# Kernel optimization log

Measured on AMD Instinct MI355X. Metric: run time of the kernel, lower is better.

The kernel has to match this reference:

```python
import jax, jax.numpy as jnp
import numpy as np

K = 20
EPS = 1e-5


def knn_idx(x, k):
    # x: (B, N, C) -> (B, N, k) indices of k nearest neighbors (incl. self)
    xx = jnp.sum(x * x, axis=-1, keepdims=True)           # (B,N,1)
    inner = -2.0 * jnp.einsum('bnc,bmc->bnm', x, x)        # (B,N,N)
    pd = -xx - inner - jnp.swapaxes(xx, 1, 2)              # negative sq dist
    _, idx = jax.lax.top_k(pd, k)                          # (B,N,k)
    return idx


def get_graph_feature(x, k=K):
    B, N, C = x.shape
    idx = knn_idx(x, k)                                    # (B,N,k)
    # gather neighbor features per batch
    feature = jax.vmap(lambda xb, ib: xb[ib])(x, idx)      # (B,N,k,C)
    xe = jnp.broadcast_to(x[:, :, None, :], (B, N, k, C))  # (B,N,k,C)
    f = jnp.concatenate([feature - xe, xe], axis=3)        # (B,N,k,2C)
    return jnp.transpose(f, (0, 3, 1, 2))                  # (B,2C,N,k)


def conv1x1(x, W, b):
    # x: (B,Cin,N,k), W: (Cout,Cin)
    return jnp.einsum('bcnk,oc->bonk', x, W) + b[None, :, None, None]


def batchnorm(x, gamma, beta):
    # training-mode BN over (B,N,k) per channel, biased variance (torch default)
    mean = jnp.mean(x, axis=(0, 2, 3), keepdims=True)
    var = jnp.var(x, axis=(0, 2, 3), keepdims=True)
    xhat = (x - mean) * jax.lax.rsqrt(var + EPS)
    return xhat * gamma[None, :, None, None] + beta[None, :, None, None]


def setup_inputs() -> dict:
    key = jax.random.key(0)
    ks = jax.random.split(key, 10)
    B, N, C = 4, 4096, 3
    x = jax.random.normal(ks[0], (B, N, C), dtype=jnp.float32)
    W1 = jax.random.normal(ks[1], (64, 2 * C), dtype=jnp.float32) * 0.1
    b1 = jnp.zeros((64,), jnp.float32)
    g1 = jnp.ones((64,), jnp.float32)
    be1 = jnp.zeros((64,), jnp.float32)
    W2 = jax.random.normal(ks[2], (128, 64), dtype=jnp.float32) * 0.1
    b2 = jnp.zeros((128,), jnp.float32)
    g2 = jnp.ones((128,), jnp.float32)
    be2 = jnp.zeros((128,), jnp.float32)
    W3 = jax.random.normal(ks[3], (128, 128), dtype=jnp.float32) * 0.1
    b3 = jnp.zeros((128,), jnp.float32)
    g3 = jnp.ones((128,), jnp.float32)
    be3 = jnp.zeros((128,), jnp.float32)
    return {"x": x, "W1": W1, "b1": b1, "g1": g1, "be1": be1,
            "W2": W2, "b2": b2, "g2": g2, "be2": be2,
            "W3": W3, "b3": b3, "g3": g3, "be3": be3}


def reference(x, W1, b1, g1, be1, W2, b2, g2, be2, W3, b3, g3, be3):
    f = get_graph_feature(x, K)                  # (B,6,N,k)
    h = jax.nn.relu(batchnorm(conv1x1(f, W1, b1), g1, be1))
    h = jax.nn.relu(batchnorm(conv1x1(h, W2, b2), g2, be2))
    h = batchnorm(conv1x1(h, W3, b3), g3, be3)
    return jnp.max(h, axis=-1)                   # (B,128,N)
```

## Files before the change

### kernel.cpp

```cpp
#include <hip/hip_runtime.h>


typedef __attribute__((ext_vector_type(8)))  short short8;
typedef __attribute__((ext_vector_type(4)))  float floatx4;

#define BATCH 4
#define NPTS  4096
#define KNN   20
#define BN_   (BATCH*NPTS)
#define CNT   (BATCH*NPTS*KNN)

__device__ __forceinline__ unsigned short f2bf(float f) {
  unsigned u = __float_as_uint(f);
  unsigned r = u + 0x7FFFu + ((u >> 16) & 1u);
  return (unsigned short)(r >> 16);
}

__device__ __forceinline__ short8 pack8(float a, float b, float c, float d,
                                        float e, float f, float g, float h) {
  short8 r;
  r[0]=(short)f2bf(a); r[1]=(short)f2bf(b); r[2]=(short)f2bf(c); r[3]=(short)f2bf(d);
  r[4]=(short)f2bf(e); r[5]=(short)f2bf(f); r[6]=(short)f2bf(g); r[7]=(short)f2bf(h);
  return r;
}

__device__ __forceinline__ unsigned mono(float f) {
  unsigned u = __float_as_uint(f);
  return u ^ ((unsigned)((int)u >> 31) | 0x80000000u);
}

__global__ void pf_prep(const float* __restrict__ x, float4* __restrict__ xp,
                        float* __restrict__ stats) {
  int pt = blockIdx.x * 256 + threadIdx.x;
  float x0 = x[pt*3+0], x1 = x[pt*3+1], x2 = x[pt*3+2];
  float xx = x0*x0 + x1*x1 + x2*x2;
  xp[pt] = make_float4(x0, x1, x2, xx);
  if (blockIdx.x == 0)
    for (int i = threadIdx.x; i < 640; i += 256) stats[i] = 0.0f;
}

__device__ __forceinline__ float sort_take20th(float v, int lane) {
  #pragma unroll
  for (int k = 2; k <= 64; k <<= 1) {
    #pragma unroll
    for (int j = k >> 1; j >= 1; j >>= 1) {
      float o = __shfl_xor(v, j);
      bool keepmax = (((lane & j) == 0) == ((lane & k) == 0));
      v = keepmax ? fmaxf(v, o) : fminf(v, o);
    }
  }
  return __shfl(v, 19);
}

__device__ __forceinline__ unsigned long long sort64_desc(unsigned long long v,
                                                          int lane) {
  #pragma unroll
  for (int k = 2; k <= 64; k <<= 1) {
    #pragma unroll
    for (int j = k >> 1; j >= 1; j >>= 1) {
      unsigned long long o = __shfl_xor(v, j);
      bool keepmax = (((lane & j) == 0) == ((lane & k) == 0));
      unsigned long long hi = v > o ? v : o;
      unsigned long long lo = v > o ? o : v;
      v = keepmax ? hi : lo;
    }
  }
  return v;
}

__global__ __launch_bounds__(256) void pf_knn(const float4* __restrict__ xp,
                                              int* __restrict__ idxb) {
  __shared__ unsigned long long lst[8][128];
  __shared__ int lcnt[8];
  const int tid  = threadIdx.x;
  const int lane = tid & 63;
  const int w    = tid >> 6;
  const int b    = blockIdx.x >> 9;
  const int nb   = (blockIdx.x & 511) * 8 + w * 2;
  const float4* xb = xp + b * NPTS;

  float4 q0 = xb[nb], q1 = xb[nb + 1];

  float mx0 = -3.0e38f, mx1 = -3.0e38f;
  for (int j0 = 0; j0 < NPTS; j0 += 64) {
    float4 c = xb[j0 + lane];
    float d0 = fmaf(q0.x,c.x, fmaf(q0.y,c.y, q0.z*c.z));
    float d1 = fmaf(q1.x,c.x, fmaf(q1.y,c.y, q1.z*c.z));
    mx0 = fmaxf(mx0, fmaf(2.f,d0,-q0.w) - c.w);
    mx1 = fmaxf(mx1, fmaf(2.f,d1,-q1.w) - c.w);
  }
  float T0 = sort_take20th(mx0, lane);
  float T1 = sort_take20th(mx1, lane);

  if (lane < 2) lcnt[w*2 + lane] = 0;
  __syncthreads();

  for (int j0 = 0; j0 < NPTS; j0 += 64) {
    float4 c = xb[j0 + lane];
    float d0 = fmaf(q0.x,c.x, fmaf(q0.y,c.y, q0.z*c.z));
    float d1 = fmaf(q1.x,c.x, fmaf(q1.y,c.y, q1.z*c.z));
    float p0 = fmaf(2.f,d0,-q0.w) - c.w;
    float p1 = fmaf(2.f,d1,-q1.w) - c.w;
    unsigned long long keybase = (unsigned long long)(4095 - (j0 + lane));
    if (p0 >= T0) {
      int o = atomicAdd(&lcnt[w*2+0], 1);
      if (o < 128) lst[w*2+0][o] = ((unsigned long long)mono(p0) << 32) | keybase;
    }
    if (p1 >= T1) {
      int o = atomicAdd(&lcnt[w*2+1], 1);
      if (o < 128) lst[w*2+1][o] = ((unsigned long long)mono(p1) << 32) | keybase;
    }
  }

  #pragma unroll 1
  for (int i = 0; i < 2; ++i) {
    const int li = w*2 + i;
    const int cn = lcnt[li];
    const int outbase = (b * NPTS + nb + i) * KNN;
    if (cn <= 64) {
      unsigned long long v = (lane < cn) ? lst[li][lane] : 0ull;
      v = sort64_desc(v, lane);
      if (lane < KNN) idxb[outbase + lane] = 4095 - (int)(v & 0xFFFFFFFFull);
    } else if (cn <= 128) {
      unsigned long long e0 = lst[li][lane];
      unsigned long long e1 = (lane + 64 < cn) ? lst[li][lane + 64] : 0ull;
      #pragma unroll 1
      for (int r = 0; r < KNN; ++r) {
        unsigned long long m = e0 > e1 ? e0 : e1;
        #pragma unroll
        for (int o = 32; o; o >>= 1) {
          unsigned long long t = __shfl_xor(m, o);
          m = t > m ? t : m;
        }
        if (lane == 0) idxb[outbase + r] = 4095 - (int)(m & 0xFFFFFFFFull);
        if (e0 == m) e0 = 0ull; else if (e1 == m) e1 = 0ull;
      }
    } else {
      const float4 qq = (i == 0) ? q0 : q1;
      unsigned long long prev = ~0ull;
      #pragma unroll 1
      for (int r = 0; r < KNN; ++r) {
        unsigned long long best = 0ull;
        for (int j0 = 0; j0 < NPTS; j0 += 64) {
          float4 c = xb[j0 + lane];
          float dd = fmaf(qq.x,c.x, fmaf(qq.y,c.y, qq.z*c.z));
          float pd = fmaf(2.f,dd,-qq.w) - c.w;
          unsigned long long key = ((unsigned long long)mono(pd) << 32) |
                                   (unsigned long long)(4095 - (j0 + lane));
          if (key < prev && key > best) best = key;
        }
        #pragma unroll
        for (int o = 32; o; o >>= 1) {
          unsigned long long t = __shfl_xor(best, o);
          best = t > best ? t : best;
        }
        if (lane == 0) idxb[outbase + r] = 4095 - (int)(best & 0xFFFFFFFFull);
        prev = best;
      }
    }
  }
}

__global__ __launch_bounds__(256) void pf_stats1(
    const float4* __restrict__ xp, const int* __restrict__ idxb,
    const float* __restrict__ W1, const float* __restrict__ b1,
    float* __restrict__ gs1, float* __restrict__ gq1) {
  __shared__ float S[64], Q[64];
  const int tid = threadIdx.x;
  const int c = tid & 63, slice = tid >> 6;
  if (tid < 64) { S[tid] = 0.f; Q[tid] = 0.f; }
  __syncthreads();
  const float wa0=W1[c*6+0], wa1=W1[c*6+1], wa2=W1[c*6+2];
  const float wb0=W1[c*6+3], wb1=W1[c*6+4], wb2=W1[c*6+5];
  const float bb = b1[c];
  float s = 0.f, q = 0.f;
  int ptbase = (blockIdx.x * 4 + slice) * 4;
  for (int u = 0; u < 4; ++u) {
    int pt = ptbase + u;
    float4 xi = xp[pt];
    int ib = (pt >> 12) << 12;
    for (int kk = 0; kk < KNN; ++kk) {
      int j = idxb[pt*KNN + kk];
      float4 xj = xp[ib + j];
      float y = bb;
      y = fmaf(wa0, xj.x - xi.x, y);
      y = fmaf(wa1, xj.y - xi.y, y);
      y = fmaf(wa2, xj.z - xi.z, y);
      y = fmaf(wb0, xi.x, y);
      y = fmaf(wb1, xi.y, y);
      y = fmaf(wb2, xi.z, y);
      s += y; q = fmaf(y, y, q);
    }
  }
  atomicAdd(&S[c], s); atomicAdd(&Q[c], q);
  __syncthreads();
  if (tid < 64) { atomicAdd(&gs1[tid], S[tid]); atomicAdd(&gq1[tid], Q[tid]); }
}

__global__ void pf_affine(const float* __restrict__ gs, const float* __restrict__ gq,
                          const float* __restrict__ gamma, const float* __restrict__ beta,
                          const float* __restrict__ bconv, int foldb, int C,
                          float* __restrict__ sc, float* __restrict__ sh) {
  int c = threadIdx.x;
  if (c < C) {
    const float inv = 1.0f / (float)CNT;
    float mean = gs[c] * inv;
    float var  = gq[c] * inv - mean * mean;
    float s = gamma[c] * rsqrtf(var + 1e-5f);
    float shift = beta[c] - mean * s;
    if (foldb) shift = fmaf(s, bconv[c], shift);
    sc[c] = s; sh[c] = shift;
  }
}

__global__ __launch_bounds__(256, 2) void pf_stats2(
    const float4* __restrict__ xp, const int* __restrict__ idxb,
    const float* __restrict__ W1, const float* __restrict__ sc1e,
    const float* __restrict__ sh1e, const float* __restrict__ W2,
    const float* __restrict__ b2,
    float* __restrict__ gs2, float* __restrict__ gq2) {
  __shared__ __align__(16) float4 XI[32];
  __shared__ __align__(16) float4 XJ[32];
  __shared__ __align__(16) unsigned short H1[32][72];
  __shared__ float SS[128], SQ[128];

  const int tid = threadIdx.x;
  const int lane = tid & 63, w = tid >> 6;
  const int chalf = w & 1, rh = w >> 1;
  const int l15 = lane & 15, quad = lane >> 4;
  const int pt0 = blockIdx.x * 32;

  if (tid < 128) { SS[tid] = 0.f; SQ[tid] = 0.f; }
  if (tid < 32)  XI[tid] = xp[pt0 + tid];

  short8 w1f[2];
  #pragma unroll
  for (int t = 0; t < 2; ++t) {
    short8 f = {0,0,0,0,0,0,0,0};
    if (quad == 0) {
      const float* p = W1 + (32*chalf + 16*t + l15) * 6;
      f = pack8(p[0],p[1],p[2],p[3],p[4],p[5],0.f,0.f);
    }
    w1f[t] = f;
  }
  float a1[2], s1[2];
  #pragma unroll
  for (int t = 0; t < 2; ++t) {
    int c = 32*chalf + 16*t + l15;
    a1[t] = sc1e[c]; s1[t] = sh1e[c];
  }
  short8 w2f[2][4];
  #pragma unroll
  for (int ks = 0; ks < 2; ++ks)
    #pragma unroll
    for (int t = 0; t < 4; ++t) {
      const float* p = W2 + (64*chalf + 16*t + l15) * 64 + 32*ks + quad*8;
      w2f[ks][t] = pack8(p[0],p[1],p[2],p[3],p[4],p[5],p[6],p[7]);
    }
  float bb2[4];
  #pragma unroll
  for (int t = 0; t < 4; ++t) bb2[t] = b2[64*chalf + 16*t + l15];

  float sum[4] = {0,0,0,0}, sq[4] = {0,0,0,0};

  for (int kk = 0; kk < KNN; ++kk) {
    if (tid < 32) {
      int pt = pt0 + tid;
      XJ[tid] = xp[((pt >> 12) << 12) + idxb[pt*KNN + kk]];
    }
    __syncthreads();
    short8 af = {0,0,0,0,0,0,0,0};
    if (quad == 0) {
      float4 xi = XI[rh*16 + l15];
      float4 xj = XJ[rh*16 + l15];
      af = pack8(xj.x-xi.x, xj.y-xi.y, xj.z-xi.z, xi.x, xi.y, xi.z, 0.f, 0.f);
    }
    floatx4 acc1[2] = {{0,0,0,0},{0,0,0,0}};
    #pragma unroll
    for (int t = 0; t < 2; ++t)
      acc1[t] = __builtin_amdgcn_mfma_f32_16x16x32_bf16(af, w1f[t], acc1[t], 0,0,0);
    #pragma unroll
    for (int t = 0; t < 2; ++t) {
      int c = 32*chalf + 16*t + l15;
      #pragma unroll
      for (int r = 0; r < 4; ++r) {
        float h = fmaxf(fmaf(a1[t], acc1[t][r], s1[t]), 0.f);
        H1[rh*16 + quad*4 + r][c] = f2bf(h);
      }
    }
    __syncthreads();
    floatx4 acc2[4] = {{0,0,0,0},{0,0,0,0},{0,0,0,0},{0,0,0,0}};
    #pragma unroll
    for (int ks = 0; ks < 2; ++ks) {
      short8 a = *(const short8*)&H1[rh*16 + l15][ks*32 + quad*8];
      #pragma unroll
      for (int t = 0; t < 4; ++t)
        acc2[t] = __builtin_amdgcn_mfma_f32_16x16x32_bf16(a, w2f[ks][t], acc2[t], 0,0,0);
    }
    #pragma unroll
    for (int t = 0; t < 4; ++t)
      #pragma unroll
      for (int r = 0; r < 4; ++r) {
        float v = acc2[t][r] + bb2[t];
        sum[t] += v; sq[t] = fmaf(v, v, sq[t]);
      }
  }
  #pragma unroll
  for (int t = 0; t < 4; ++t) {
    float s = sum[t], z = sq[t];
    s += __shfl_xor(s, 16); z += __shfl_xor(z, 16);
    s += __shfl_xor(s, 32); z += __shfl_xor(z, 32);
    if (quad == 0) {
      int c = 64*chalf + 16*t + l15;
      atomicAdd(&SS[c], s); atomicAdd(&SQ[c], z);
    }
  }
  __syncthreads();
  if (tid < 128) { atomicAdd(&gs2[tid], SS[tid]); atomicAdd(&gq2[tid], SQ[tid]); }
}

__global__ __launch_bounds__(256, 2) void pf_main(
    const float4* __restrict__ xp, const int* __restrict__ idxb,
    const float* __restrict__ W1, const float* __restrict__ sc1e,
    const float* __restrict__ sh1e, const float* __restrict__ W2,
    const float* __restrict__ sc2e, const float* __restrict__ shm2,
    const float* __restrict__ W3, const float* __restrict__ b3,
    float* __restrict__ gs3, float* __restrict__ gq3,
    float* __restrict__ maxv) {
  __shared__ __align__(16) float4 XI[32];
  __shared__ __align__(16) float4 XJ[32];
  __shared__ __align__(16) unsigned short H1[32][72];
  __shared__ __align__(16) unsigned short H2[32][136];
  __shared__ float SS[128], SQ[128];

  const int tid = threadIdx.x;
  const int lane = tid & 63, w = tid >> 6;
  const int chalf = w & 1, rh = w >> 1;
  const int l15 = lane & 15, quad = lane >> 4;
  const int pt0 = blockIdx.x * 32;

  if (tid < 128) { SS[tid] = 0.f; SQ[tid] = 0.f; }
  if (tid < 32)  XI[tid] = xp[pt0 + tid];

  short8 w1f[2];
  #pragma unroll
  for (int t = 0; t < 2; ++t) {
    short8 f = {0,0,0,0,0,0,0,0};
    if (quad == 0) {
      const float* p = W1 + (32*chalf + 16*t + l15) * 6;
      f = pack8(p[0],p[1],p[2],p[3],p[4],p[5],0.f,0.f);
    }
    w1f[t] = f;
  }
  float a1[2], s1[2];
  #pragma unroll
  for (int t = 0; t < 2; ++t) {
    int c = 32*chalf + 16*t + l15;
    a1[t] = sc1e[c]; s1[t] = sh1e[c];
  }
  short8 w2f[2][4];
  #pragma unroll
  for (int ks = 0; ks < 2; ++ks)
    #pragma unroll
    for (int t = 0; t < 4; ++t) {
      const float* p = W2 + (64*chalf + 16*t + l15) * 64 + 32*ks + quad*8;
      w2f[ks][t] = pack8(p[0],p[1],p[2],p[3],p[4],p[5],p[6],p[7]);
    }
  float a2[4], s2[4], bb3[4];
  #pragma unroll
  for (int t = 0; t < 4; ++t) {
    int c = 64*chalf + 16*t + l15;
    a2[t] = sc2e[c]; s2[t] = shm2[c]; bb3[t] = b3[c];
  }
  short8 w3f[4][4];
  #pragma unroll
  for (int ks = 0; ks < 4; ++ks)
    #pragma unroll
    for (int t = 0; t < 4; ++t) {
      const float* p = W3 + (64*chalf + 16*t + l15) * 128 + 32*ks + quad*8;
      w3f[ks][t] = pack8(p[0],p[1],p[2],p[3],p[4],p[5],p[6],p[7]);
    }

  float sum[4] = {0,0,0,0}, sq[4] = {0,0,0,0};
  float mx[4][4];
  #pragma unroll
  for (int t = 0; t < 4; ++t)
    #pragma unroll
    for (int r = 0; r < 4; ++r) mx[t][r] = -3.0e38f;

  for (int kk = 0; kk < KNN; ++kk) {
    if (tid < 32) {
      int pt = pt0 + tid;
      XJ[tid] = xp[((pt >> 12) << 12) + idxb[pt*KNN + kk]];
    }
    __syncthreads();
    short8 af = {0,0,0,0,0,0,0,0};
    if (quad == 0) {
      float4 xi = XI[rh*16 + l15];
      float4 xj = XJ[rh*16 + l15];
      af = pack8(xj.x-xi.x, xj.y-xi.y, xj.z-xi.z, xi.x, xi.y, xi.z, 0.f, 0.f);
    }
    floatx4 acc1[2] = {{0,0,0,0},{0,0,0,0}};
    #pragma unroll
    for (int t = 0; t < 2; ++t)
      acc1[t] = __builtin_amdgcn_mfma_f32_16x16x32_bf16(af, w1f[t], acc1[t], 0,0,0);
    #pragma unroll
    for (int t = 0; t < 2; ++t) {
      int c = 32*chalf + 16*t + l15;
      #pragma unroll
      for (int r = 0; r < 4; ++r) {
        float h = fmaxf(fmaf(a1[t], acc1[t][r], s1[t]), 0.f);
        H1[rh*16 + quad*4 + r][c] = f2bf(h);
      }
    }
    __syncthreads();
    floatx4 acc2[4] = {{0,0,0,0},{0,0,0,0},{0,0,0,0},{0,0,0,0}};
    #pragma unroll
    for (int ks = 0; ks < 2; ++ks) {
      short8 a = *(const short8*)&H1[rh*16 + l15][ks*32 + quad*8];
      #pragma unroll
      for (int t = 0; t < 4; ++t)
        acc2[t] = __builtin_amdgcn_mfma_f32_16x16x32_bf16(a, w2f[ks][t], acc2[t], 0,0,0);
    }
    #pragma unroll
    for (int t = 0; t < 4; ++t) {
      int c = 64*chalf + 16*t + l15;
      #pragma unroll
      for (int r = 0; r < 4; ++r) {
        float h = fmaxf(fmaf(a2[t], acc2[t][r], s2[t]), 0.f);
        H2[rh*16 + quad*4 + r][c] = f2bf(h);
      }
    }
    __syncthreads();
    floatx4 acc3[4] = {{0,0,0,0},{0,0,0,0},{0,0,0,0},{0,0,0,0}};
    #pragma unroll
    for (int ks = 0; ks < 4; ++ks) {
      short8 a = *(const short8*)&H2[rh*16 + l15][ks*32 + quad*8];
      #pragma unroll
      for (int t = 0; t < 4; ++t)
        acc3[t] = __builtin_amdgcn_mfma_f32_16x16x32_bf16(a, w3f[ks][t], acc3[t], 0,0,0);
    }
    #pragma unroll
    for (int t = 0; t < 4; ++t)
      #pragma unroll
      for (int r = 0; r < 4; ++r) {
        float v = acc3[t][r] + bb3[t];
        sum[t] += v; sq[t] = fmaf(v, v, sq[t]);
        mx[t][r] = fmaxf(mx[t][r], v);
      }
  }
  #pragma unroll
  for (int t = 0; t < 4; ++t) {
    int c = 64*chalf + 16*t + l15;
    #pragma unroll
    for (int r = 0; r < 4; ++r) {
      int row = rh*16 + quad*4 + r;
      maxv[(pt0 + row)*128 + c] = mx[t][r];
    }
  }
  #pragma unroll
  for (int t = 0; t < 4; ++t) {
    float s = sum[t], z = sq[t];
    s += __shfl_xor(s, 16); z += __shfl_xor(z, 16);
    s += __shfl_xor(s, 32); z += __shfl_xor(z, 32);
    if (quad == 0) {
      int c = 64*chalf + 16*t + l15;
      atomicAdd(&SS[c], s); atomicAdd(&SQ[c], z);
    }
  }
  __syncthreads();
  if (tid < 128) { atomicAdd(&gs3[tid], SS[tid]); atomicAdd(&gq3[tid], SQ[tid]); }
}

__global__ __launch_bounds__(256) void pf_out(
    const float* __restrict__ maxv, const float* __restrict__ sc3,
    const float* __restrict__ sh3, float* __restrict__ out) {
  __shared__ float T[128][65];
  __shared__ float SC[128], SH[128];
  const int tid = threadIdx.x;
  const int b  = blockIdx.x >> 6;
  const int n0 = (blockIdx.x & 63) * 64;
  if (tid < 128) { SC[tid] = sc3[tid]; SH[tid] = sh3[tid]; }
  __syncthreads();
  const float4* mv4 = (const float4*)maxv;
  #pragma unroll
  for (int r = 0; r < 8; ++r) {
    int fid = r * 256 + tid;
    int nl = fid >> 5, c4 = fid & 31;
    float4 v = mv4[(b*NPTS + n0 + nl)*32 + c4];
    int c = c4 * 4;
    T[c+0][nl] = fmaf(SC[c+0], v.x, SH[c+0]);
    T[c+1][nl] = fmaf(SC[c+1], v.y, SH[c+1]);
    T[c+2][nl] = fmaf(SC[c+2], v.z, SH[c+2]);
    T[c+3][nl] = fmaf(SC[c+3], v.w, SH[c+3]);
  }
  __syncthreads();
  #pragma unroll
  for (int r = 0; r < 8; ++r) {
    int fid = r * 256 + tid;
    int c = fid >> 4, nq = fid & 15;
    float4 o;
    o.x = T[c][nq*4+0]; o.y = T[c][nq*4+1];
    o.z = T[c][nq*4+2]; o.w = T[c][nq*4+3];
    *(float4*)(out + (size_t)b*128*NPTS + (size_t)c*NPTS + n0 + nq*4) = o;
  }
}

extern "C" void kernel_launch(void* const* d_in, const int* in_sizes, int n_in,
                              void* d_out, int out_size, void* d_ws, size_t ws_size,
                              hipStream_t stream) {
  const float* x   = (const float*)d_in[0];
  const float* W1  = (const float*)d_in[1];
  const float* b1  = (const float*)d_in[2];
  const float* g1  = (const float*)d_in[3];
  const float* be1 = (const float*)d_in[4];
  const float* W2  = (const float*)d_in[5];
  const float* b2  = (const float*)d_in[6];
  const float* g2  = (const float*)d_in[7];
  const float* be2 = (const float*)d_in[8];
  const float* W3  = (const float*)d_in[9];
  const float* b3  = (const float*)d_in[10];
  const float* g3  = (const float*)d_in[11];
  const float* be3 = (const float*)d_in[12];
  float* out = (float*)d_out;

  char* p = (char*)d_ws;
  float4* xp  = (float4*)p;            p += (size_t)BN_ * 16;
  int*    idxb= (int*)p;               p += (size_t)BN_ * KNN * 4;
  float*  stats = (float*)p;           p += 640 * 4;
  float*  aff   = (float*)p;           p += 640 * 4;
  float*  maxv  = (float*)p;

  float *gs1 = stats,       *gq1 = stats + 64;
  float *gs2 = stats + 128, *gq2 = stats + 256;
  float *gs3 = stats + 384, *gq3 = stats + 512;
  float *sc1e = aff,        *sh1e = aff + 64;
  float *sc2e = aff + 128,  *shm2 = aff + 256;
  float *sc3  = aff + 384,  *sh3  = aff + 512;

  pf_prep  <<<64,   256, 0, stream>>>(x, xp, stats);
  pf_knn   <<<2048, 256, 0, stream>>>(xp, idxb);
  pf_stats1<<<1024, 256, 0, stream>>>(xp, idxb, W1, b1, gs1, gq1);
  pf_affine<<<1,    64,  0, stream>>>(gs1, gq1, g1, be1, b1, 1, 64, sc1e, sh1e);
  pf_stats2<<<512,  256, 0, stream>>>(xp, idxb, W1, sc1e, sh1e, W2, b2, gs2, gq2);
  pf_affine<<<1,    128, 0, stream>>>(gs2, gq2, g2, be2, b2, 1, 128, sc2e, shm2);
  pf_main  <<<512,  256, 0, stream>>>(xp, idxb, W1, sc1e, sh1e, W2, sc2e, shm2,
                                      W3, b3, gs3, gq3, maxv);
  pf_affine<<<1,    128, 0, stream>>>(gs3, gq3, g3, be3, b3, 0, 128, sc3, sh3);
  pf_out   <<<256,  256, 0, stream>>>(maxv, sc3, sh3, out);
}
```

Before: 250.6 us.

## Compute BN1 stats from input moments, split k across blocks, fold BN scales

Layer-1 BatchNorm statistics now come from the 27 first and second moments of the 6-dim edge features, combined with W1 in a tiny affine kernel, replacing the per-channel gather pass. The stats2 and main kernels work on 16 points per block instead of 32 and can split the 20 neighbours over two blocks, each writing a partial max plane that pf_out merges. This raises the block count and occupancy. They also fold the BN scale into the bf16 weights, start the accumulators at the shift or bias, and double-buffer the neighbour gather. The risks are rounding from pre-scaled bf16 weights and extra maxv traffic when the workspace allows the split.

Result: slower. 328.3 us (+31.0%).

```diff
diff --git a/kernel.cpp b/kernel.cpp
--- a/kernel.cpp
+++ b/kernel.cpp
@@ -161,40 +161,70 @@
   }
 }
 
-__global__ __launch_bounds__(256) void pf_stats1(
+__global__ __launch_bounds__(256) void pf_mom(
     const float4* __restrict__ xp, const int* __restrict__ idxb,
-    const float* __restrict__ W1, const float* __restrict__ b1,
-    float* __restrict__ gs1, float* __restrict__ gq1) {
-  __shared__ float S[64], Q[64];
+    float* __restrict__ mom) {
+  __shared__ float M[27];
   const int tid = threadIdx.x;
-  const int c = tid & 63, slice = tid >> 6;
-  if (tid < 64) { S[tid] = 0.f; Q[tid] = 0.f; }
-  __syncthreads();
-  const float wa0=W1[c*6+0], wa1=W1[c*6+1], wa2=W1[c*6+2];
-  const float wb0=W1[c*6+3], wb1=W1[c*6+4], wb2=W1[c*6+5];
-  const float bb = b1[c];
-  float s = 0.f, q = 0.f;
-  int ptbase = (blockIdx.x * 4 + slice) * 4;
-  for (int u = 0; u < 4; ++u) {
-    int pt = ptbase + u;
-    float4 xi = xp[pt];
-    int ib = (pt >> 12) << 12;
-    for (int kk = 0; kk < KNN; ++kk) {
-      int j = idxb[pt*KNN + kk];
-      float4 xj = xp[ib + j];
-      float y = bb;
-      y = fmaf(wa0, xj.x - xi.x, y);
-      y = fmaf(wa1, xj.y - xi.y, y);
-      y = fmaf(wa2, xj.z - xi.z, y);
-      y = fmaf(wb0, xi.x, y);
-      y = fmaf(wb1, xi.y, y);
-      y = fmaf(wb2, xi.z, y);
-      s += y; q = fmaf(y, y, q);
-    }
-  }
-  atomicAdd(&S[c], s); atomicAdd(&Q[c], q);
-  __syncthreads();
-  if (tid < 64) { atomicAdd(&gs1[tid], S[tid]); atomicAdd(&gq1[tid], Q[tid]); }
+  if (tid < 27) M[tid] = 0.f;
+  __syncthreads();
+  const int gid = blockIdx.x * 256 + tid;
+  const int pt = gid >> 1;
+  const int kk0 = (gid & 1) * 10;
+  const float4 xi = xp[pt];
+  const int ib = pt & ~(NPTS - 1);
+  float a[27];
+  #pragma unroll
+  for (int i = 0; i < 27; ++i) a[i] = 0.f;
+  #pragma unroll 1
+  for (int u = 0; u < 10; ++u) {
+    int j = idxb[pt*KNN + kk0 + u];
+    float4 xj = xp[ib + j];
+    float f[6] = {xj.x - xi.x, xj.y - xi.y, xj.z - xi.z, xi.x, xi.y, xi.z};
+    int idx = 6;
+    #pragma unroll
+    for (int i1 = 0; i1 < 6; ++i1) {
+      a[i1] += f[i1];
+      #pragma unroll
+      for (int i2 = i1; i2 < 6; ++i2) { a[idx] = fmaf(f[i1], f[i2], a[idx]); ++idx; }
+    }
+  }
+  #pragma unroll
+  for (int i = 0; i < 27; ++i) atomicAdd(&M[i], a[i]);
+  __syncthreads();
+  if (tid < 27) atomicAdd(&mom[tid], M[tid]);
+}
+
+__global__ void pf_affine1m(const float* __restrict__ mom,
+                            const float* __restrict__ W1, const float* __restrict__ b1,
+                            const float* __restrict__ g1, const float* __restrict__ be1,
+                            float* __restrict__ sc, float* __restrict__ sh) {
+  int c = threadIdx.x;
+  float wv[6];
+  #pragma unroll
+  for (int i = 0; i < 6; ++i) wv[i] = W1[c*6 + i];
+  float b = b1[c];
+  float S1 = b * (float)CNT;
+  float Q  = b * b * (float)CNT;
+  int idx = 6;
+  #pragma unroll
+  for (int i = 0; i < 6; ++i) {
+    float m1 = mom[i];
+    S1 += wv[i] * m1;
+    Q  += 2.0f * b * wv[i] * m1;
+    #pragma unroll
+    for (int j = i; j < 6; ++j) {
+      float coef = (i == j) ? 1.0f : 2.0f;
+      Q += coef * wv[i] * wv[j] * mom[idx];
+      ++idx;
+    }
+  }
+  const float inv = 1.0f / (float)CNT;
+  float mean = S1 * inv;
+  float var  = Q * inv - mean * mean;
+  float s = g1[c] * rsqrtf(var + 1e-5f);
+  sc[c] = s;
+  sh[c] = be1[c] - mean * s + s * b;
 }
 
 __global__ void pf_affine(const float* __restrict__ gs, const float* __restrict__ gq,
@@ -213,105 +243,96 @@
   }
 }
 
-__global__ __launch_bounds__(256, 2) void pf_stats2(
+__global__ __launch_bounds__(256, 4) void pf_stats2(
     const float4* __restrict__ xp, const int* __restrict__ idxb,
     const float* __restrict__ W1, const float* __restrict__ sc1e,
     const float* __restrict__ sh1e, const float* __restrict__ W2,
-    const float* __restrict__ b2,
+    const float* __restrict__ b2, int kshift, int kpb,
     float* __restrict__ gs2, float* __restrict__ gq2) {
-  __shared__ __align__(16) float4 XI[32];
-  __shared__ __align__(16) float4 XJ[32];
-  __shared__ __align__(16) unsigned short H1[32][72];
+  __shared__ __align__(16) float4 XI[16];
+  __shared__ __align__(16) float4 XJ[2][16];
+  __shared__ __align__(16) unsigned short H1[2][16][72];
   __shared__ float SS[128], SQ[128];
 
   const int tid = threadIdx.x;
   const int lane = tid & 63, w = tid >> 6;
-  const int chalf = w & 1, rh = w >> 1;
   const int l15 = lane & 15, quad = lane >> 4;
-  const int pt0 = blockIdx.x * 32;
+  const int pg = blockIdx.x >> kshift;
+  const int ks0 = blockIdx.x & ((1 << kshift) - 1);
+  const int kk0 = ks0 * kpb;
+  const int pt0 = pg * 16;
+  const int ib = pt0 & ~(NPTS - 1);
 
   if (tid < 128) { SS[tid] = 0.f; SQ[tid] = 0.f; }
-  if (tid < 32)  XI[tid] = xp[pt0 + tid];
-
-  short8 w1f[2];
+  if (tid < 16) XI[tid] = xp[pt0 + tid];
+  if (tid < 16) XJ[0][tid] = xp[ib + idxb[(pt0 + tid)*KNN + kk0]];
+
+  const int c1 = 16*w + l15;
+  const float s1 = sh1e[c1];
+  short8 w1f = {0,0,0,0,0,0,0,0};
+  {
+    float a1 = sc1e[c1];
+    if (quad == 0) {
+      const float* p = W1 + c1*6;
+      w1f = pack8(p[0]*a1,p[1]*a1,p[2]*a1,p[3]*a1,p[4]*a1,p[5]*a1,0.f,0.f);
+    }
+  }
+  short8 w2f[2][2];
+  float bb2[2];
   #pragma unroll
   for (int t = 0; t < 2; ++t) {
-    short8 f = {0,0,0,0,0,0,0,0};
-    if (quad == 0) {
-      const float* p = W1 + (32*chalf + 16*t + l15) * 6;
-      f = pack8(p[0],p[1],p[2],p[3],p[4],p[5],0.f,0.f);
-    }
-    w1f[t] = f;
-  }
-  float a1[2], s1[2];
-  #pragma unroll
-  for (int t = 0; t < 2; ++t) {
-    int c = 32*chalf + 16*t + l15;
-    a1[t] = sc1e[c]; s1[t] = sh1e[c];
-  }
-  short8 w2f[2][4];
-  #pragma unroll
-  for (int ks = 0; ks < 2; ++ks)
-    #pragma unroll
-    for (int t = 0; t < 4; ++t) {
-      const float* p = W2 + (64*chalf + 16*t + l15) * 64 + 32*ks + quad*8;
-      w2f[ks][t] = pack8(p[0],p[1],p[2],p[3],p[4],p[5],p[6],p[7]);
-    }
-  float bb2[4];
-  #pragma unroll
-  for (int t = 0; t < 4; ++t) bb2[t] = b2[64*chalf + 16*t + l15];
-
-  float sum[4] = {0,0,0,0}, sq[4] = {0,0,0,0};
-
-  for (int kk = 0; kk < KNN; ++kk) {
-    if (tid < 32) {
-      int pt = pt0 + tid;
-      XJ[tid] = xp[((pt >> 12) << 12) + idxb[pt*KNN + kk]];
-    }
-    __syncthreads();
+    int c = 32*w + 16*t + l15;
+    bb2[t] = b2[c];
+    #pragma unroll
+    for (int ksl = 0; ksl < 2; ++ksl) {
+      const float* p = W2 + c*64 + 32*ksl + quad*8;
+      w2f[ksl][t] = pack8(p[0],p[1],p[2],p[3],p[4],p[5],p[6],p[7]);
+    }
+  }
+
+  float sum[2] = {0,0}, sq[2] = {0,0};
+  __syncthreads();
+
+  for (int it = 0; it < kpb; ++it) {
+    const int cur = it & 1;
     short8 af = {0,0,0,0,0,0,0,0};
     if (quad == 0) {
-      float4 xi = XI[rh*16 + l15];
-      float4 xj = XJ[rh*16 + l15];
+      float4 xi = XI[l15];
+      float4 xj = XJ[cur][l15];
       af = pack8(xj.x-xi.x, xj.y-xi.y, xj.z-xi.z, xi.x, xi.y, xi.z, 0.f, 0.f);
     }
-    floatx4 acc1[2] = {{0,0,0,0},{0,0,0,0}};
+    if (tid < 16 && it + 1 < kpb)
+      XJ[1-cur][tid] = xp[ib + idxb[(pt0 + tid)*KNN + kk0 + it + 1]];
+    floatx4 acc1 = {s1, s1, s1, s1};
+    acc1 = __builtin_amdgcn_mfma_f32_16x16x32_bf16(af, w1f, acc1, 0,0,0);
+    #pragma unroll
+    for (int r = 0; r < 4; ++r)
+      H1[cur][quad*4 + r][c1] = f2bf(fmaxf(acc1[r], 0.f));
+    __syncthreads();
+    floatx4 acc2[2] = {{bb2[0],bb2[0],bb2[0],bb2[0]},
+                       {bb2[1],bb2[1],bb2[1],bb2[1]}};
+    #pragma unroll
+    for (int ksl = 0; ksl < 2; ++ksl) {
+      short8 a = *(const short8*)&H1[cur][l15][ksl*32 + quad*8];
+      #pragma unroll
+      for (int t = 0; t < 2; ++t)
+        acc2[t] = __builtin_amdgcn_mfma_f32_16x16x32_bf16(a, w2f[ksl][t], acc2[t], 0,0,0);
+    }
     #pragma unroll
     for (int t = 0; t < 2; ++t)
-      acc1[t] = __builtin_amdgcn_mfma_f32_16x16x32_bf16(af, w1f[t], acc1[t], 0,0,0);
-    #pragma unroll
-    for (int t = 0; t < 2; ++t) {
-      int c = 32*chalf + 16*t + l15;
       #pragma unroll
       for (int r = 0; r < 4; ++r) {
-        float h = fmaxf(fmaf(a1[t], acc1[t][r], s1[t]), 0.f);
-        H1[rh*16 + quad*4 + r][c] = f2bf(h);
-      }
-    }
-    __syncthreads();
-    floatx4 acc2[4] = {{0,0,0,0},{0,0,0,0},{0,0,0,0},{0,0,0,0}};
-    #pragma unroll
-    for (int ks = 0; ks < 2; ++ks) {
-      short8 a = *(const short8*)&H1[rh*16 + l15][ks*32 + quad*8];
-      #pragma unroll
-      for (int t = 0; t < 4; ++t)
-        acc2[t] = __builtin_amdgcn_mfma_f32_16x16x32_bf16(a, w2f[ks][t], acc2[t], 0,0,0);
-    }
-    #pragma unroll
-    for (int t = 0; t < 4; ++t)
-      #pragma unroll
-      for (int r = 0; r < 4; ++r) {
-        float v = acc2[t][r] + bb2[t];
+        float v = acc2[t][r];
         sum[t] += v; sq[t] = fmaf(v, v, sq[t]);
       }
   }
   #pragma unroll
-  for (int t = 0; t < 4; ++t) {
+  for (int t = 0; t < 2; ++t) {
     float s = sum[t], z = sq[t];
     s += __shfl_xor(s, 16); z += __shfl_xor(z, 16);
     s += __shfl_xor(s, 32); z += __shfl_xor(z, 32);
     if (quad == 0) {
-      int c = 64*chalf + 16*t + l15;
+      int c = 32*w + 16*t + l15;
       atomicAdd(&SS[c], s); atomicAdd(&SQ[c], z);
     }
   }
@@ -319,152 +340,145 @@
   if (tid < 128) { atomicAdd(&gs2[tid], SS[tid]); atomicAdd(&gq2[tid], SQ[tid]); }
 }
 
-__global__ __launch_bounds__(256, 2) void pf_main(
+__global__ __launch_bounds__(256, 4) void pf_main(
     const float4* __restrict__ xp, const int* __restrict__ idxb,
     const float* __restrict__ W1, const float* __restrict__ sc1e,
     const float* __restrict__ sh1e, const float* __restrict__ W2,
     const float* __restrict__ sc2e, const float* __restrict__ shm2,
     const float* __restrict__ W3, const float* __restrict__ b3,
+    int kshift, int kpb,
     float* __restrict__ gs3, float* __restrict__ gq3,
     float* __restrict__ maxv) {
-  __shared__ __align__(16) float4 XI[32];
-  __shared__ __align__(16) float4 XJ[32];
-  __shared__ __align__(16) unsigned short H1[32][72];
-  __shared__ __align__(16) unsigned short H2[32][136];
+  __shared__ __align__(16) float4 XI[16];
+  __shared__ __align__(16) float4 XJ[2][16];
+  __shared__ __align__(16) unsigned short H1[16][72];
+  __shared__ __align__(16) unsigned short H2[16][136];
   __shared__ float SS[128], SQ[128];
 
   const int tid = threadIdx.x;
   const int lane = tid & 63, w = tid >> 6;
-  const int chalf = w & 1, rh = w >> 1;
   const int l15 = lane & 15, quad = lane >> 4;
-  const int pt0 = blockIdx.x * 32;
+  const int pg = blockIdx.x >> kshift;
+  const int ks0 = blockIdx.x & ((1 << kshift) - 1);
+  const int kk0 = ks0 * kpb;
+  const int pt0 = pg * 16;
+  const int ib = pt0 & ~(NPTS - 1);
 
   if (tid < 128) { SS[tid] = 0.f; SQ[tid] = 0.f; }
-  if (tid < 32)  XI[tid] = xp[pt0 + tid];
-
-  short8 w1f[2];
+  if (tid < 16) XI[tid] = xp[pt0 + tid];
+  if (tid < 16) XJ[0][tid] = xp[ib + idxb[(pt0 + tid)*KNN + kk0]];
+
+  const int c1 = 16*w + l15;
+  const float s1 = sh1e[c1];
+  short8 w1f = {0,0,0,0,0,0,0,0};
+  {
+    float a1 = sc1e[c1];
+    if (quad == 0) {
+      const float* p = W1 + c1*6;
+      w1f = pack8(p[0]*a1,p[1]*a1,p[2]*a1,p[3]*a1,p[4]*a1,p[5]*a1,0.f,0.f);
+    }
+  }
+  short8 w2f[2][2];
+  float s2v[2];
   #pragma unroll
   for (int t = 0; t < 2; ++t) {
-    short8 f = {0,0,0,0,0,0,0,0};
-    if (quad == 0) {
-      const float* p = W1 + (32*chalf + 16*t + l15) * 6;
-      f = pack8(p[0],p[1],p[2],p[3],p[4],p[5],0.f,0.f);
-    }
-    w1f[t] = f;
-  }
-  float a1[2], s1[2];
+    int c = 32*w + 16*t + l15;
+    float a2 = sc2e[c];
+    s2v[t] = shm2[c];
+    #pragma unroll
+    for (int ksl = 0; ksl < 2; ++ksl) {
+      const float* p = W2 + c*64 + 32*ksl + quad*8;
+      w2f[ksl][t] = pack8(p[0]*a2,p[1]*a2,p[2]*a2,p[3]*a2,p[4]*a2,p[5]*a2,p[6]*a2,p[7]*a2);
+    }
+  }
+  short8 w3f[4][2];
+  float bb3[2];
   #pragma unroll
   for (int t = 0; t < 2; ++t) {
-    int c = 32*chalf + 16*t + l15;
-    a1[t] = sc1e[c]; s1[t] = sh1e[c];
-  }
-  short8 w2f[2][4];
-  #pragma unroll
-  for (int ks = 0; ks < 2; ++ks)
-    #pragma unroll
-    for (int t = 0; t < 4; ++t) {
-      const float* p = W2 + (64*chalf + 16*t + l15) * 64 + 32*ks + quad*8;
-      w2f[ks][t] = pack8(p[0],p[1],p[2],p[3],p[4],p[5],p[6],p[7]);
-    }
-  float a2[4], s2[4], bb3[4];
-  #pragma unroll
-  for (int t = 0; t < 4; ++t) {
-    int c = 64*chalf + 16*t + l15;
-    a2[t] = sc2e[c]; s2[t] = shm2[c]; bb3[t] = b3[c];
-  }
-  short8 w3f[4][4];
-  #pragma unroll
-  for (int ks = 0; ks < 4; ++ks)
-    #pragma unroll
-    for (int t = 0; t < 4; ++t) {
-      const float* p = W3 + (64*chalf + 16*t + l15) * 128 + 32*ks + quad*8;
-      w3f[ks][t] = pack8(p[0],p[1],p[2],p[3],p[4],p[5],p[6],p[7]);
-    }
-
-  float sum[4] = {0,0,0,0}, sq[4] = {0,0,0,0};
-  float mx[4][4];
-  #pragma unroll
-  for (int t = 0; t < 4; ++t)
+    int c = 32*w + 16*t + l15;
+    bb3[t] = b3[c];
+    #pragma unroll
+    for (int ksl = 0; ksl < 4; ++ksl) {
+      const float* p = W3 + c*128 + 32*ksl + quad*8;
+      w3f[ksl][t] = pack8(p[0],p[1],p[2],p[3],p[4],p[5],p[6],p[7]);
+    }
+  }
+
+  float sum[2] = {0,0}, sq[2] = {0,0};
+  float mx[2][4];
+  #pragma unroll
+  for (int t = 0; t < 2; ++t)
     #pragma unroll
     for (int r = 0; r < 4; ++r) mx[t][r] = -3.0e38f;
 
-  for (int kk = 0; kk < KNN; ++kk) {
-    if (tid < 32) {
-      int pt = pt0 + tid;
-      XJ[tid] = xp[((pt >> 12) << 12) + idxb[pt*KNN + kk]];
-    }
-    __syncthreads();
+  __syncthreads();
+
+  for (int it = 0; it < kpb; ++it) {
+    const int cur = it & 1;
     short8 af = {0,0,0,0,0,0,0,0};
     if (quad == 0) {
-      float4 xi = XI[rh*16 + l15];
-      float4 xj = XJ[rh*16 + l15];
+      float4 xi = XI[l15];
+      float4 xj = XJ[cur][l15];
       af = pack8(xj.x-xi.x, xj.y-xi.y, xj.z-xi.z, xi.x, xi.y, xi.z, 0.f, 0.f);
     }
-    floatx4 acc1[2] = {{0,0,0,0},{0,0,0,0}};
+    if (tid < 16 && it + 1 < kpb)
+      XJ[1-cur][tid] = xp[ib + idxb[(pt0 + tid)*KNN + kk0 + it + 1]];
+    floatx4 acc1 = {s1, s1, s1, s1};
+    acc1 = __builtin_amdgcn_mfma_f32_16x16x32_bf16(af, w1f, acc1, 0,0,0);
+    #pragma unroll
+    for (int r = 0; r < 4; ++r)
+      H1[quad*4 + r][c1] = f2bf(fmaxf(acc1[r], 0.f));
+    __syncthreads();
+    floatx4 acc2[2] = {{s2v[0],s2v[0],s2v[0],s2v[0]},
+                       {s2v[1],s2v[1],s2v[1],s2v[1]}};
+    #pragma unroll
+    for (int ksl = 0; ksl < 2; ++ksl) {
+      short8 a = *(const short8*)&H1[l15][ksl*32 + quad*8];
+      #pragma unroll
+      for (int t = 0; t < 2; ++t)
+        acc2[t] = __builtin_amdgcn_mfma_f32_16x16x32_bf16(a, w2f[ksl][t], acc2[t], 0,0,0);
+    }
+    #pragma unroll
+    for (int t = 0; t < 2; ++t) {
+      int c = 32*w + 16*t + l15;
+      #pragma unroll
+      for (int r = 0; r < 4; ++r)
+        H2[quad*4 + r][c] = f2bf(fmaxf(acc2[t][r], 0.f));
+    }
+    __syncthreads();
+    floatx4 acc3[2] = {{bb3[0],bb3[0],bb3[0],bb3[0]},
+                       {bb3[1],bb3[1],bb3[1],bb3[1]}};
+    #pragma unroll
+    for (int ksl = 0; ksl < 4; ++ksl) {
+      short8 a = *(const short8*)&H2[l15][ksl*32 + quad*8];
+      #pragma unroll
+      for (int t = 0; t < 2; ++t)
+        acc3[t] = __builtin_amdgcn_mfma_f32_16x16x32_bf16(a, w3f[ksl][t], acc3[t], 0,0,0);
+    }
     #pragma unroll
     for (int t = 0; t < 2; ++t)
-      acc1[t] = __builtin_amdgcn_mfma_f32_16x16x32_bf16(af, w1f[t], acc1[t], 0,0,0);
-    #pragma unroll
-    for (int t = 0; t < 2; ++t) {
-      int c = 32*chalf + 16*t + l15;
       #pragma unroll
       for (int r = 0; r < 4; ++r) {
-        float h = fmaxf(fmaf(a1[t], acc1[t][r], s1[t]), 0.f);
-        H1[rh*16 + quad*4 + r][c] = f2bf(h);
-      }
-    }
-    __syncthreads();
-    floatx4 acc2[4] = {{0,0,0,0},{0,0,0,0},{0,0,0,0},{0,0,0,0}};
-    #pragma unroll
-    for (int ks = 0; ks < 2; ++ks) {
-      short8 a = *(const short8*)&H1[rh*16 + l15][ks*32 + quad*8];
-      #pragma unroll
-      for (int t = 0; t < 4; ++t)
-        acc2[t] = __builtin_amdgcn_mfma_f32_16x16x32_bf16(a, w2f[ks][t], acc2[t], 0,0,0);
-    }
-    #pragma unroll
-    for (int t = 0; t < 4; ++t) {
-      int c = 64*chalf + 16*t + l15;
-      #pragma unroll
-      for (int r = 0; r < 4; ++r) {
-        float h = fmaxf(fmaf(a2[t], acc2[t][r], s2[t]), 0.f);
-        H2[rh*16 + quad*4 + r][c] = f2bf(h);
-      }
-    }
-    __syncthreads();
-    floatx4 acc3[4] = {{0,0,0,0},{0,0,0,0},{0,0,0,0},{0,0,0,0}};
-    #pragma unroll
-    for (int ks = 0; ks < 4; ++ks) {
-      short8 a = *(const short8*)&H2[rh*16 + l15][ks*32 + quad*8];
-      #pragma unroll
-      for (int t = 0; t < 4; ++t)
-        acc3[t] = __builtin_amdgcn_mfma_f32_16x16x32_bf16(a, w3f[ks][t], acc3[t], 0,0,0);
-    }
-    #pragma unroll
-    for (int t = 0; t < 4; ++t)
-      #pragma unroll
-      for (int r = 0; r < 4; ++r) {
-        float v = acc3[t][r] + bb3[t];
+        float v = acc3[t][r];
         sum[t] += v; sq[t] = fmaf(v, v, sq[t]);
         mx[t][r] = fmaxf(mx[t][r], v);
       }
   }
-  #pragma unroll
-  for (int t = 0; t < 4; ++t) {
-    int c = 64*chalf + 16*t + l15;
-    #pragma unroll
-    for (int r = 0; r < 4; ++r) {
-      int row = rh*16 + quad*4 + r;
-      maxv[(pt0 + row)*128 + c] = mx[t][r];
-    }
-  }
-  #pragma unroll
-  for (int t = 0; t < 4; ++t) {
+  float* mp = maxv + (size_t)ks0 * BN_ * 128;
+  #pragma unroll
+  for (int t = 0; t < 2; ++t) {
+    int c = 32*w + 16*t + l15;
+    #pragma unroll
+    for (int r = 0; r < 4; ++r)
+      mp[(pt0 + quad*4 + r)*128 + c] = mx[t][r];
+  }
+  #pragma unroll
+  for (int t = 0; t < 2; ++t) {
     float s = sum[t], z = sq[t];
     s += __shfl_xor(s, 16); z += __shfl_xor(z, 16);
     s += __shfl_xor(s, 32); z += __shfl_xor(z, 32);
     if (quad == 0) {
-      int c = 64*chalf + 16*t + l15;
+      int c = 32*w + 16*t + l15;
       atomicAdd(&SS[c], s); atomicAdd(&SQ[c], z);
     }
   }
@@ -473,8 +487,9 @@
 }
 
 __global__ __launch_bounds__(256) void pf_out(
-    const float* __restrict__ maxv, const float* __restrict__ sc3,
-    const float* __restrict__ sh3, float* __restrict__ out) {
+    const float* __restrict__ maxv, int nspl,
+    const float* __restrict__ sc3, const float* __restrict__ sh3,
+    float* __restrict__ out) {
   __shared__ float T[128][65];
   __shared__ float SC[128], SH[128];
   const int tid = threadIdx.x;
@@ -488,6 +503,11 @@
     int fid = r * 256 + tid;
     int nl = fid >> 5, c4 = fid & 31;
     float4 v = mv4[(b*NPTS + n0 + nl)*32 + c4];
+    if (nspl == 2) {
+      float4 v2 = mv4[524288 + (b*NPTS + n0 + nl)*32 + c4];
+      v.x = fmaxf(v.x, v2.x); v.y = fmaxf(v.y, v2.y);
+      v.z = fmaxf(v.z, v2.z); v.w = fmaxf(v.w, v2.w);
+    }
     int c = c4 * 4;
     T[c+0][nl] = fmaf(SC[c+0], v.x, SH[c+0]);
     T[c+1][nl] = fmaf(SC[c+1], v.y, SH[c+1]);
@@ -525,27 +545,35 @@
   float* out = (float*)d_out;
 
   char* p = (char*)d_ws;
-  float4* xp  = (float4*)p;            p += (size_t)BN_ * 16;
-  int*    idxb= (int*)p;               p += (size_t)BN_ * KNN * 4;
-  float*  stats = (float*)p;           p += 640 * 4;
-  float*  aff   = (float*)p;           p += 640 * 4;
-  float*  maxv  = (float*)p;
-
-  float *gs1 = stats,       *gq1 = stats + 64;
+  float4* xp   = (float4*)(p);
+  int*    idxb = (int*)(p + 262144);
+  float*  stats= (float*)(p + 1573864 - 1000);
+  stats        = (float*)(p + 262144 + 1310720);
+  float*  aff  = (float*)(p + 262144 + 1310720 + 2560);
+  float*  maxv = (float*)(p + 262144 + 1310720 + 2560 + 2560);
+
+  const size_t plane = (size_t)BN_ * 128 * 4;
+  const size_t base  = 262144 + 1310720 + 2560 + 2560;
+  const int nspl  = (ws_size >= base + 2 * plane) ? 2 : 1;
+  const int kshift = nspl - 1;
+  const int kpb    = KNN / nspl;
+
+  float *mom = stats;
   float *gs2 = stats + 128, *gq2 = stats + 256;
   float *gs3 = stats + 384, *gq3 = stats + 512;
   float *sc1e = aff,        *sh1e = aff + 64;
   float *sc2e = aff + 128,  *shm2 = aff + 256;
   float *sc3  = aff + 384,  *sh3  = aff + 512;
 
-  pf_prep  <<<64,   256, 0, stream>>>(x, xp, stats);
-  pf_knn   <<<2048, 256, 0, stream>>>(xp, idxb);
-  pf_stats1<<<1024, 256, 0, stream>>>(xp, idxb, W1, b1, gs1, gq1);
-  pf_affine<<<1,    64,  0, stream>>>(gs1, gq1, g1, be1, b1, 1, 64, sc1e, sh1e);
-  pf_stats2<<<512,  256, 0, stream>>>(xp, idxb, W1, sc1e, sh1e, W2, b2, gs2, gq2);
-  pf_affine<<<1,    128, 0, stream>>>(gs2, gq2, g2, be2, b2, 1, 128, sc2e, shm2);
-  pf_main  <<<512,  256, 0, stream>>>(xp, idxb, W1, sc1e, sh1e, W2, sc2e, shm2,
-                                      W3, b3, gs3, gq3, maxv);
-  pf_affine<<<1,    128, 0, stream>>>(gs3, gq3, g3, be3, b3, 0, 128, sc3, sh3);
-  pf_out   <<<256,  256, 0, stream>>>(maxv, sc3, sh3, out);
-}
+  pf_prep    <<<64,   256, 0, stream>>>(x, xp, stats);
+  pf_knn     <<<2048, 256, 0, stream>>>(xp, idxb);
+  pf_mom     <<<128,  256, 0, stream>>>(xp, idxb, mom);
+  pf_affine1m<<<1,    64,  0, stream>>>(mom, W1, b1, g1, be1, sc1e, sh1e);
+  pf_stats2  <<<1024*nspl, 256, 0, stream>>>(xp, idxb, W1, sc1e, sh1e, W2, b2,
+                                             kshift, kpb, gs2, gq2);
+  pf_affine  <<<1,    128, 0, stream>>>(gs2, gq2, g2, be2, b2, 1, 128, sc2e, shm2);
+  pf_main    <<<1024*nspl, 256, 0, stream>>>(xp, idxb, W1, sc1e, sh1e, W2, sc2e, shm2,
+                                             W3, b3, kshift, kpb, gs3, gq3, maxv);
+  pf_affine  <<<1,    128, 0, stream>>>(gs3, gq3, g3, be3, b3, 0, 128, sc3, sh3);
+  pf_out     <<<256,  256, 0, stream>>>(maxv, nspl, sc3, sh3, out);
+}
```
